# Kernel tuning notes

Hardware: AMD Instinct MI355X
Metric: run time of the kernel (lower is better)

The kernel has to match this reference:

```python
import jax, jax.numpy as jnp
import numpy as np

N, E, G, L = 50000, 800000, 256, 3
D, NF, EF, OUT = 300, 128, 16, 128
BN_EPS = 1e-5


def setup_inputs() -> dict:
    key = jax.random.key(0)
    ks = jax.random.split(key, 24)
    s = 0.02
    inp = {
        "node_feat": jax.random.normal(ks[0], (N, NF), jnp.float32),
        "edge_feat": jax.random.normal(ks[1], (E, EF), jnp.float32),
        "src": jax.random.randint(ks[2], (E,), 0, N),
        "dst": jax.random.randint(ks[3], (E,), 0, N),
        "graph_ids": jnp.sort(jax.random.randint(ks[4], (N,), 0, G)),
        "num_graphs": G,
        # encoder params
        "node_W": jax.random.normal(ks[5], (NF, D), jnp.float32) * s,
        "node_b": jnp.zeros((D,), jnp.float32),
        # per-layer edge encoders [L, EF, D]
        "edge_W": jax.random.normal(ks[6], (L, EF, D), jnp.float32) * s,
        "edge_b": jnp.zeros((L, D), jnp.float32),
        # per-layer GINEConv MLP: Linear(D,2D) BN ReLU Linear(2D,D) BN
        "W1": jax.random.normal(ks[7], (L, D, 2 * D), jnp.float32) * s,
        "b1": jnp.zeros((L, 2 * D), jnp.float32),
        "g1": jnp.ones((L, 2 * D), jnp.float32),
        "beta1": jnp.zeros((L, 2 * D), jnp.float32),
        "W2": jax.random.normal(ks[8], (L, 2 * D, D), jnp.float32) * s,
        "b2": jnp.zeros((L, D), jnp.float32),
        "g2": jnp.ones((L, D), jnp.float32),
        "beta2": jnp.zeros((L, D), jnp.float32),
        # prediction head
        "pred_W": jax.random.normal(ks[9], (D, OUT), jnp.float32) * s,
        "pred_b": jnp.zeros((OUT,), jnp.float32),
    }
    return inp


def _bn(x, g, b):
    # BatchNorm1d in training mode: biased batch statistics
    m = jnp.mean(x, axis=0)
    v = jnp.var(x, axis=0)
    return (x - m) * jax.lax.rsqrt(v + BN_EPS) * g + b


def reference(node_feat, edge_feat, src, dst, graph_ids, num_graphs,
              node_W, node_b, edge_W, edge_b,
              W1, b1, g1, beta1, W2, b2, g2, beta2,
              pred_W, pred_b):
    n_nodes = node_feat.shape[0]
    n_layers = edge_W.shape[0]
    hn = node_feat @ node_W + node_b  # [N, D]
    for l in range(n_layers):
        he = edge_feat @ edge_W[l] + edge_b[l]            # [E, D]
        msg = jax.nn.relu(hn[src] + he)                   # gather + edge fuse
        agg = jax.ops.segment_sum(msg, dst, num_segments=n_nodes)
        h = hn + agg                                      # (1+eps)*h + agg, eps=0
        h = jax.nn.relu(_bn(h @ W1[l] + b1[l], g1[l], beta1[l]))
        h = _bn(h @ W2[l] + b2[l], g2[l], beta2[l])
        hn = jax.nn.relu(h) if l != n_layers - 1 else h   # dropout p=0 -> identity
    # AvgPooling over nodes per graph
    cnt = jax.ops.segment_sum(jnp.ones((n_nodes, 1), hn.dtype), graph_ids,
                              num_segments=num_graphs)
    hg = jax.ops.segment_sum(hn, graph_ids, num_segments=num_graphs)
    hg = hg / jnp.maximum(cnt, 1.0)
    return hg @ pred_W + pred_b  # [G, OUT]
```

## Files before the change

kernel.cpp:

```cpp
#include <hip/hip_runtime.h>

#define N_NODES 50000
#define N_EDGES 800000
#define N_GRAPHS 256
#define N_LAYERS 3
#define DIM 300
#define NFEAT 128
#define EFEAT 16
#define OUTD 128
#define BN_EPS 1e-5f

typedef __attribute__((ext_vector_type(8))) short bfrag8;
typedef __attribute__((ext_vector_type(4))) float facc4;
typedef __attribute__((ext_vector_type(4))) unsigned short us4;
typedef __attribute__((ext_vector_type(8))) unsigned short us8;

__device__ __forceinline__ unsigned short f2bf(float f) {
    unsigned u = __float_as_uint(f);
    unsigned r = ((u >> 16) & 1u) + 0x7fffu;
    return (unsigned short)((u + r) >> 16);
}
__device__ __forceinline__ float bf2f(unsigned short h) {
    return __uint_as_float(((unsigned)h) << 16);
}
__device__ __forceinline__ void split2(float v, unsigned short& h, unsigned short& l) {
    h = f2bf(v);
    l = f2bf(v - bf2f(h));
}

__device__ __forceinline__ void load_lds16(const void* gsrc, void* ldsdst) {
    __builtin_amdgcn_global_load_lds(
        (const __attribute__((address_space(1))) unsigned int*)gsrc,
        (__attribute__((address_space(3))) unsigned int*)ldsdst,
        16, 0, 0);
}

#define MFMA16(a, b, c) __builtin_amdgcn_mfma_f32_16x16x32_bf16(a, b, c, 0, 0, 0)

__global__ __launch_bounds__(256) void tobf4(
    const float* __restrict__ x, unsigned short* __restrict__ H, int n4)
{
    int i = blockIdx.x * 256 + threadIdx.x;
    if (i >= n4) return;
    float4 v = ((const float4*)x)[i];
    us4 h;
    h.x = f2bf(v.x); h.y = f2bf(v.y); h.z = f2bf(v.z); h.w = f2bf(v.w);
    ((us4*)H)[i] = h;
}

__global__ __launch_bounds__(256) void conv_wt(
    const float* __restrict__ W, unsigned short* __restrict__ H,
    unsigned short* __restrict__ L, int K, int N, int Kp, int Np)
{
    int idx = blockIdx.x * 256 + threadIdx.x;
    if (idx >= Np * Kp) return;
    int n = idx / Kp;
    int k = idx - n * Kp;
    float v = (n < N && k < K) ? W[(size_t)k * N + n] : 0.f;
    unsigned short h, l;
    split2(v, h, l);
    H[idx] = h;
    L[idx] = l;
}

__global__ __launch_bounds__(256, 2) void gemm_pp(
    const unsigned short* __restrict__ Ah,
    const unsigned short* __restrict__ Bth, const unsigned short* __restrict__ Btl,
    const float* __restrict__ bias, float* __restrict__ C,
    int M, int N, int Kp, float* __restrict__ stats)
{
    __shared__ unsigned short lds[12288];
    const int tid = threadIdx.x;
    const int lane = tid & 63;
    const int w = tid >> 6;
    const int m0 = blockIdx.y * 128;
    const int n0 = blockIdx.x * 128;
    const int wm = (w & 1) * 64;
    const int wn = (w >> 1) * 64;

    const int srow = lane >> 2;
    const int scol = (lane & 3) * 8;

    const unsigned short* gp[6];
    unsigned loff[6];
#pragma unroll
    for (int i = 0; i < 6; ++i) {
        int c = w * 6 + i;
        const unsigned short* pl = (c < 8) ? Ah : (c < 16) ? Bth : Btl;
        int rowg;
        if (c < 8) {
            rowg = m0 + (c & 7) * 16 + srow;
            rowg = min(rowg, M - 1);
        } else {
            rowg = n0 + (c & 7) * 16 + srow;
        }
        gp[i] = pl + (size_t)rowg * Kp + scol;
        loff[i] = c * 512;
    }

    facc4 acc[4][4];
    facc4 zero = {0.f, 0.f, 0.f, 0.f};
#pragma unroll
    for (int i = 0; i < 4; ++i)
#pragma unroll
        for (int j = 0; j < 4; ++j) acc[i][j] = zero;

    const int fr = lane & 15;
    const int fq = (lane >> 4) * 8;

    for (int k0 = 0; k0 < Kp; k0 += 32) {
#pragma unroll
        for (int i = 0; i < 6; ++i) {
            load_lds16(gp[i], &lds[loff[i]]);
            gp[i] += 32;
        }
        __syncthreads();

        bfrag8 ah[4], bh[4], bl[4];
#pragma unroll
        for (int t = 0; t < 4; ++t) {
            int ar = wm + t * 16 + fr;
            ah[t] = *(const bfrag8*)&lds[ar * 32 + fq];
            int br = wn + t * 16 + fr;
            bh[t] = *(const bfrag8*)&lds[4096 + br * 32 + fq];
            bl[t] = *(const bfrag8*)&lds[8192 + br * 32 + fq];
        }
#pragma unroll
        for (int i = 0; i < 4; ++i)
#pragma unroll
            for (int j = 0; j < 4; ++j) {
                acc[i][j] = MFMA16(ah[i], bh[j], acc[i][j]);
                acc[i][j] = MFMA16(ah[i], bl[j], acc[i][j]);
            }
        __syncthreads();
    }

#pragma unroll
    for (int i = 0; i < 4; ++i)
#pragma unroll
        for (int j = 0; j < 4; ++j) {
            int col = n0 + wn + j * 16 + (lane & 15);
            if (col >= N) continue;
            float bv = bias[col];
#pragma unroll
            for (int r = 0; r < 4; ++r) {
                int row = m0 + wm + i * 16 + (lane >> 4) * 4 + r;
                if (row < M)
                    C[(size_t)row * N + col] = acc[i][j][r] + bv;
            }
        }

    if (stats != nullptr) {
#pragma unroll
        for (int j = 0; j < 4; ++j) {
            int col = n0 + wn + j * 16 + (lane & 15);
            float cs = 0.f, cq = 0.f;
            if (col < N) {
                float bv = bias[col];
#pragma unroll
                for (int i = 0; i < 4; ++i)
#pragma unroll
                    for (int r = 0; r < 4; ++r) {
                        int row = m0 + wm + i * 16 + (lane >> 4) * 4 + r;
                        if (row < M) {
                            float y = acc[i][j][r] + bv;
                            cs += y;
                            cq = fmaf(y, y, cq);
                        }
                    }
            }
            cs += __shfl_xor(cs, 16, 64); cq += __shfl_xor(cq, 16, 64);
            cs += __shfl_xor(cs, 32, 64); cq += __shfl_xor(cq, 32, 64);
            if ((lane >> 4) == 0 && col < N) {
                atomicAdd(&stats[col], cs);
                atomicAdd(&stats[N + col], cq);
            }
        }
    }
}

__global__ __launch_bounds__(256, 2) void gemm_af(
    const float* __restrict__ A, const unsigned short* __restrict__ Bth,
    const unsigned short* __restrict__ Btl, const float* __restrict__ bias,
    float* __restrict__ C, int M, int N, int K, int Kp,
    const float* __restrict__ abn, float* __restrict__ stats)
{
    __shared__ unsigned short lds[12288];
    const int tid = threadIdx.x;
    const int lane = tid & 63;
    const int w = tid >> 6;
    const int m0 = blockIdx.y * 128;
    const int n0 = blockIdx.x * 128;
    const int wm = (w & 1) * 64;
    const int wn = (w >> 1) * 64;

    const int srow = lane >> 2;
    const int scol = (lane & 3) * 8;

    const unsigned short* gpb[4];
    unsigned loffb[4];
#pragma unroll
    for (int i = 0; i < 4; ++i) {
        int c = w * 4 + i;
        const unsigned short* pl = (c < 8) ? Bth : Btl;
        int rowg = n0 + (c & 7) * 16 + srow;
        gpb[i] = pl + (size_t)rowg * Kp + scol;
        loffb[i] = 4096 + c * 512;
    }

    facc4 acc[4][4];
    facc4 zero = {0.f, 0.f, 0.f, 0.f};
#pragma unroll
    for (int i = 0; i < 4; ++i)
#pragma unroll
        for (int j = 0; j < 4; ++j) acc[i][j] = zero;

    const int fr = lane & 15;
    const int fq = (lane >> 4) * 8;

    for (int k0 = 0; k0 < Kp; k0 += 32) {
#pragma unroll
        for (int i = 0; i < 4; ++i) {
            load_lds16(gpb[i], &lds[loffb[i]]);
            gpb[i] += 32;
        }
#pragma unroll
        for (int i = 0; i < 4; ++i) {
            int idx = tid + i * 256;
            int row = idx >> 3;
            int q4 = idx & 7;
            int rg = min(m0 + row, M - 1);
            int kk = k0 + q4 * 4;
            us4 h;
            if (kk < K) {
                float4 v = *(const float4*)&A[(size_t)rg * K + kk];
                float4 sa = *(const float4*)&abn[kk];
                float4 sb = *(const float4*)&abn[K + kk];
                h.x = f2bf(fmaxf(fmaf(v.x, sa.x, sb.x), 0.f));
                h.y = f2bf(fmaxf(fmaf(v.y, sa.y, sb.y), 0.f));
                h.z = f2bf(fmaxf(fmaf(v.z, sa.z, sb.z), 0.f));
                h.w = f2bf(fmaxf(fmaf(v.w, sa.w, sb.w), 0.f));
            } else {
                h.x = 0; h.y = 0; h.z = 0; h.w = 0;
            }
            *(us4*)&lds[row * 32 + q4 * 4] = h;
        }
        __syncthreads();

        bfrag8 ah[4], bh[4], bl[4];
#pragma unroll
        for (int t = 0; t < 4; ++t) {
            int ar = wm + t * 16 + fr;
            ah[t] = *(const bfrag8*)&lds[ar * 32 + fq];
            int br = wn + t * 16 + fr;
            bh[t] = *(const bfrag8*)&lds[4096 + br * 32 + fq];
            bl[t] = *(const bfrag8*)&lds[8192 + br * 32 + fq];
        }
#pragma unroll
        for (int i = 0; i < 4; ++i)
#pragma unroll
            for (int j = 0; j < 4; ++j) {
                acc[i][j] = MFMA16(ah[i], bh[j], acc[i][j]);
                acc[i][j] = MFMA16(ah[i], bl[j], acc[i][j]);
            }
        __syncthreads();
    }

#pragma unroll
    for (int i = 0; i < 4; ++i)
#pragma unroll
        for (int j = 0; j < 4; ++j) {
            int col = n0 + wn + j * 16 + (lane & 15);
            if (col >= N) continue;
            float bv = bias[col];
#pragma unroll
            for (int r = 0; r < 4; ++r) {
                int row = m0 + wm + i * 16 + (lane >> 4) * 4 + r;
                if (row < M)
                    C[(size_t)row * N + col] = acc[i][j][r] + bv;
            }
        }

    if (stats != nullptr) {
#pragma unroll
        for (int j = 0; j < 4; ++j) {
            int col = n0 + wn + j * 16 + (lane & 15);
            float cs = 0.f, cq = 0.f;
            if (col < N) {
                float bv = bias[col];
#pragma unroll
                for (int i = 0; i < 4; ++i)
#pragma unroll
                    for (int r = 0; r < 4; ++r) {
                        int row = m0 + wm + i * 16 + (lane >> 4) * 4 + r;
                        if (row < M) {
                            float y = acc[i][j][r] + bv;
                            cs += y;
                            cq = fmaf(y, y, cq);
                        }
                    }
            }
            cs += __shfl_xor(cs, 16, 64); cq += __shfl_xor(cq, 16, 64);
            cs += __shfl_xor(cs, 32, 64); cq += __shfl_xor(cq, 32, 64);
            if ((lane >> 4) == 0 && col < N) {
                atomicAdd(&stats[col], cs);
                atomicAdd(&stats[N + col], cq);
            }
        }
    }
}

__global__ __launch_bounds__(256) void csr_count(const int* __restrict__ dst, int* __restrict__ P)
{
    int e = blockIdx.x * 256 + threadIdx.x;
    if (e < N_EDGES) atomicAdd(&P[dst[e] + 1], 1);
}

__global__ __launch_bounds__(1024) void csr_scan(int* __restrict__ P)
{
    __shared__ int part[1024];
    const int t = threadIdx.x;
    const int CH = 49;
    int i0 = t * CH;
    int s = 0;
    for (int i = i0; i < i0 + CH; ++i) {
        if (i <= N_NODES) { s += P[i]; P[i] = s; }
    }
    part[t] = s;
    __syncthreads();
    if (t == 0) {
        int run = 0;
        for (int k = 0; k < 1024; ++k) { int tmp = part[k]; part[k] = run; run += tmp; }
    }
    __syncthreads();
    int off = part[t];
    for (int i = i0; i < i0 + CH; ++i) {
        if (i <= N_NODES) P[i] += off;
    }
}

__global__ __launch_bounds__(256) void csr_fill(
    const int* __restrict__ dst, int* __restrict__ P, int* __restrict__ eids)
{
    int e = blockIdx.x * 256 + threadIdx.x;
    if (e < N_EDGES) {
        int pos = atomicAdd(&P[dst[e]], 1);
        eids[pos] = e;
    }
}

__global__ __launch_bounds__(256) void edge_pack_bf(
    const int* __restrict__ src, const int* __restrict__ eids,
    const float* __restrict__ edge_feat, int* __restrict__ es,
    unsigned short* __restrict__ efsb)
{
    int j = blockIdx.x * 256 + threadIdx.x;
    if (j >= N_EDGES) return;
    int e = eids[j];
    es[j] = src[e];
    const float* sp = edge_feat + (size_t)e * EFEAT;
    us8 o0, o1;
#pragma unroll
    for (int k = 0; k < 8; ++k) {
        o0[k] = f2bf(sp[k]);
        o1[k] = f2bf(sp[8 + k]);
    }
    *(us8*)&efsb[(size_t)j * EFEAT] = o0;
    *(us8*)&efsb[(size_t)j * EFEAT + 8] = o1;
}

__global__ __launch_bounds__(256) void gather_agg7(
    const float* __restrict__ hn, const unsigned short* __restrict__ efsb,
    const int* __restrict__ es, const int* __restrict__ P,
    const float* __restrict__ eW, const float* __restrict__ eb,
    unsigned short* __restrict__ aggH)
{
    const int v = blockIdx.x * 4 + (threadIdx.x >> 6);
    if (v >= N_NODES) return;
    const int lane = threadIdx.x & 63;

    float wr[EFEAT][5];
    float acc[5];
    float ebv[5];
#pragma unroll
    for (int c = 0; c < 5; ++c) {
        int d = lane + 64 * c;
        bool dv = d < DIM;
        acc[c] = dv ? hn[(size_t)v * DIM + d] : 0.f;
        ebv[c] = dv ? eb[d] : 0.f;
#pragma unroll
        for (int k = 0; k < EFEAT; ++k)
            wr[k][c] = dv ? eW[k * DIM + d] : 0.f;
    }

    const int j0 = (v == 0) ? 0 : P[v - 1];
    const int j1 = P[v];

    int j = j0;
    for (; j + 4 <= j1; j += 4) {
        int s0 = __builtin_amdgcn_readfirstlane(es[j]);
        int s1 = __builtin_amdgcn_readfirstlane(es[j + 1]);
        int s2 = __builtin_amdgcn_readfirstlane(es[j + 2]);
        int s3 = __builtin_amdgcn_readfirstlane(es[j + 3]);
        const float* __restrict__ h0 = hn + (size_t)s0 * DIM;
        const float* __restrict__ h1 = hn + (size_t)s1 * DIM;
        const float* __restrict__ h2p = hn + (size_t)s2 * DIM;
        const float* __restrict__ h3 = hn + (size_t)s3 * DIM;
        float hv[4][5];
#pragma unroll
        for (int c = 0; c < 5; ++c) {
            int d = lane + 64 * c;
            bool dv = d < DIM;
            hv[0][c] = dv ? h0[d] : 0.f;
            hv[1][c] = dv ? h1[d] : 0.f;
            hv[2][c] = dv ? h2p[d] : 0.f;
            hv[3][c] = dv ? h3[d] : 0.f;
        }
        us8 pk[4][2];
#pragma unroll
        for (int u = 0; u < 4; ++u) {
            pk[u][0] = *(const us8*)&efsb[(size_t)(j + u) * EFEAT];
            pk[u][1] = *(const us8*)&efsb[(size_t)(j + u) * EFEAT + 8];
        }
#pragma unroll
        for (int u = 0; u < 4; ++u) {
            float ef[EFEAT];
#pragma unroll
            for (int k = 0; k < 8; ++k) {
                ef[k] = bf2f(pk[u][0][k]);
                ef[8 + k] = bf2f(pk[u][1][k]);
            }
#pragma unroll
            for (int c = 0; c < 5; ++c) {
                float he = ebv[c];
#pragma unroll
                for (int k = 0; k < EFEAT; ++k) he = fmaf(ef[k], wr[k][c], he);
                acc[c] += fmaxf(hv[u][c] + he, 0.f);
            }
        }
    }
    for (; j < j1; ++j) {
        int s = __builtin_amdgcn_readfirstlane(es[j]);
        const float* __restrict__ hp = hn + (size_t)s * DIM;
        float hv[5];
#pragma unroll
        for (int c = 0; c < 5; ++c) {
            int d = lane + 64 * c;
            hv[c] = (d < DIM) ? hp[d] : 0.f;
        }
        us8 p0 = *(const us8*)&efsb[(size_t)j * EFEAT];
        us8 p1 = *(const us8*)&efsb[(size_t)j * EFEAT + 8];
        float ef[EFEAT];
#pragma unroll
        for (int k = 0; k < 8; ++k) {
            ef[k] = bf2f(p0[k]);
            ef[8 + k] = bf2f(p1[k]);
        }
#pragma unroll
        for (int c = 0; c < 5; ++c) {
            float he = ebv[c];
#pragma unroll
            for (int k = 0; k < EFEAT; ++k) he = fmaf(ef[k], wr[k][c], he);
            acc[c] += fmaxf(hv[c] + he, 0.f);
        }
    }

#pragma unroll
    for (int c = 0; c < 5; ++c)
        aggH[(size_t)v * 320 + lane + 64 * c] = f2bf(acc[c]);
}

__global__ __launch_bounds__(256) void bn_finalize(
    const float* __restrict__ stats, const float* __restrict__ g,
    const float* __restrict__ beta, float* __restrict__ ab, int C)
{
    int c = blockIdx.x * 256 + threadIdx.x;
    if (c >= C) return;
    const float invN = 1.f / (float)N_NODES;
    float m = stats[c] * invN;
    float v = stats[C + c] * invN - m * m;
    float a = g[c] * rsqrtf(v + BN_EPS);
    ab[c] = a;
    ab[C + c] = beta[c] - m * a;
}

__global__ __launch_bounds__(256) void bn_apply(
    const float* __restrict__ x, const float* __restrict__ ab,
    float* __restrict__ y, int total4, int C, int relu)
{
    int i = blockIdx.x * 256 + threadIdx.x;
    if (i >= total4) return;
    float4 v = ((const float4*)x)[i];
    int c = (i << 2) % C;
    const float* a = ab + c;
    const float* bb = ab + C + c;
    float4 r;
    r.x = fmaf(v.x, a[0], bb[0]);
    r.y = fmaf(v.y, a[1], bb[1]);
    r.z = fmaf(v.z, a[2], bb[2]);
    r.w = fmaf(v.w, a[3], bb[3]);
    if (relu) {
        r.x = fmaxf(r.x, 0.f); r.y = fmaxf(r.y, 0.f);
        r.z = fmaxf(r.z, 0.f); r.w = fmaxf(r.w, 0.f);
    }
    ((float4*)y)[i] = r;
}

__global__ __launch_bounds__(256) void pool_seg_bn(
    const float* __restrict__ h2, const int* __restrict__ gid,
    const float* __restrict__ ab, float* __restrict__ hg)
{
    const int g = blockIdx.x;
    int lo = 0, hi = N_NODES;
    while (lo < hi) { int mid = (lo + hi) >> 1; if (gid[mid] < g) lo = mid + 1; else hi = mid; }
    int lo2 = lo, hi2 = N_NODES;
    while (lo2 < hi2) { int mid = (lo2 + hi2) >> 1; if (gid[mid] < g + 1) lo2 = mid + 1; else hi2 = mid; }
    const float inv = 1.f / fmaxf((float)(lo2 - lo), 1.f);
    for (int d = threadIdx.x; d < DIM; d += 256) {
        float s = 0.f;
        for (int r = lo; r < lo2; ++r) s += h2[(size_t)r * DIM + d];
        hg[(size_t)g * DIM + d] = fmaf(s * inv, ab[d], ab[DIM + d]);
    }
}

#define TS 64
#define BK 16
#define ASP 68

__global__ __launch_bounds__(256) void sgemm_bias(
    const float* __restrict__ A, const float* __restrict__ B,
    const float* __restrict__ bias, float* __restrict__ C,
    int M, int Ncol, int K)
{
    __shared__ float As[BK][ASP];
    __shared__ float Bs[BK][TS];
    const int tid = threadIdx.x;
    const int bm = blockIdx.x * TS;
    const int bn = blockIdx.y * TS;
    const int tm = (tid >> 4) * 4;
    const int tn = (tid & 15) * 4;
    float acc[4][4] = {};

    for (int k0 = 0; k0 < K; k0 += BK) {
#pragma unroll
        for (int i = 0; i < 4; ++i) {
            int idx = tid + i * 256;
            int m = idx >> 4;
            int k = idx & 15;
            int row = bm + m, kk = k0 + k;
            float v = 0.f;
            if (row < M && kk < K) v = A[(size_t)row * K + kk];
            As[k][m] = v;
        }
#pragma unroll
        for (int i = 0; i < 4; ++i) {
            int idx = tid + i * 256;
            int k = idx >> 6;
            int n = idx & 63;
            int col = bn + n, kk = k0 + k;
            float v = 0.f;
            if (col < Ncol && kk < K) v = B[(size_t)kk * Ncol + col];
            Bs[k][n] = v;
        }
        __syncthreads();
#pragma unroll
        for (int k = 0; k < BK; ++k) {
            float4 av = *(const float4*)&As[k][tm];
            float4 bv = *(const float4*)&Bs[k][tn];
            float a4[4] = {av.x, av.y, av.z, av.w};
            float b4[4] = {bv.x, bv.y, bv.z, bv.w};
#pragma unroll
            for (int i = 0; i < 4; ++i)
#pragma unroll
                for (int j = 0; j < 4; ++j)
                    acc[i][j] = fmaf(a4[i], b4[j], acc[i][j]);
        }
        __syncthreads();
    }

#pragma unroll
    for (int i = 0; i < 4; ++i) {
        int row = bm + tm + i;
        if (row >= M) continue;
#pragma unroll
        for (int j = 0; j < 4; ++j) {
            int col = bn + tn + j;
            if (col < Ncol)
                C[(size_t)row * Ncol + col] = acc[i][j] + bias[col];
        }
    }
}

extern "C" void kernel_launch(void* const* d_in, const int* in_sizes, int n_in,
                              void* d_out, int out_size, void* d_ws, size_t ws_size,
                              hipStream_t stream)
{
    const float* node_feat = (const float*)d_in[0];
    const float* edge_feat = (const float*)d_in[1];
    const int*   src       = (const int*)d_in[2];
    const int*   dst       = (const int*)d_in[3];
    const int*   gid       = (const int*)d_in[4];
    const float* node_W = (const float*)d_in[6];
    const float* node_b = (const float*)d_in[7];
    const float* edge_W = (const float*)d_in[8];
    const float* edge_b = (const float*)d_in[9];
    const float* W1  = (const float*)d_in[10];
    const float* b1  = (const float*)d_in[11];
    const float* g1  = (const float*)d_in[12];
    const float* be1 = (const float*)d_in[13];
    const float* W2  = (const float*)d_in[14];
    const float* b2  = (const float*)d_in[15];
    const float* g2  = (const float*)d_in[16];
    const float* be2 = (const float*)d_in[17];
    const float* pred_W = (const float*)d_in[18];
    const float* pred_b = (const float*)d_in[19];
    float* out = (float*)d_out;

    char* base = (char*)d_ws;
    float* hn            = (float*)(base + 0);
    float* h2            = hn;
    float* x1            = (float*)(base + 60000000);
    unsigned short* nfH  = (unsigned short*)x1;
    unsigned short* aggH = (unsigned short*)(base + 180000000);
    int*   es            = (int*)(base + 212000000);
    unsigned short* efsb = (unsigned short*)(base + 215200000);
    unsigned short* wtH  = (unsigned short*)(base + 244000000);
    unsigned short* wtL  = (unsigned short*)(base + 244500000);
    int*   eids          = (int*)(base + 245000000);
    int*   P             = (int*)(base + 248200000);
    float* stats         = (float*)(base + 248400016);
    float* ab            = (float*)(base + 248407216);
    float* hg            = (float*)(base + 248414416);
    float* stats2        = stats + 1200;
    float* ab2           = ab + 1200;

    dim3 blk(256);

    tobf4<<<dim3((N_NODES * NFEAT / 4 + 255) / 256), blk, 0, stream>>>(
        node_feat, nfH, N_NODES * NFEAT / 4);
    conv_wt<<<dim3((384 * 128 + 255) / 256), blk, 0, stream>>>(
        node_W, wtH, wtL, NFEAT, DIM, 128, 384);
    gemm_pp<<<dim3(3, 391), blk, 0, stream>>>(
        nfH, wtH, wtL, node_b, hn, N_NODES, DIM, 128, nullptr);

    hipMemsetAsync(P, 0, (N_NODES + 1) * sizeof(int), stream);
    csr_count<<<dim3((N_EDGES + 255) / 256), blk, 0, stream>>>(dst, P);
    csr_scan<<<dim3(1), dim3(1024), 0, stream>>>(P);
    csr_fill<<<dim3((N_EDGES + 255) / 256), blk, 0, stream>>>(dst, P, eids);
    edge_pack_bf<<<dim3((N_EDGES + 255) / 256), blk, 0, stream>>>(
        src, eids, edge_feat, es, efsb);

    for (int l = 0; l < N_LAYERS; ++l) {
        gather_agg7<<<dim3((N_NODES + 3) / 4), blk, 0, stream>>>(
            hn, efsb, es, P,
            edge_W + (size_t)l * EFEAT * DIM, edge_b + (size_t)l * DIM, aggH);

        hipMemsetAsync(stats, 0, 1800 * sizeof(float), stream);

        conv_wt<<<dim3((640 * 320 + 255) / 256), blk, 0, stream>>>(
            W1 + (size_t)l * DIM * 2 * DIM, wtH, wtL, DIM, 2 * DIM, 320, 640);
        gemm_pp<<<dim3(5, 391), blk, 0, stream>>>(
            aggH, wtH, wtL, b1 + (size_t)l * 2 * DIM, x1,
            N_NODES, 2 * DIM, 320, stats);
        bn_finalize<<<dim3(3), blk, 0, stream>>>(
            stats, g1 + (size_t)l * 2 * DIM, be1 + (size_t)l * 2 * DIM, ab, 2 * DIM);

        conv_wt<<<dim3((384 * 608 + 255) / 256), blk, 0, stream>>>(
            W2 + (size_t)l * 2 * DIM * DIM, wtH, wtL, 2 * DIM, DIM, 608, 384);
        gemm_af<<<dim3(3, 391), blk, 0, stream>>>(
            x1, wtH, wtL, b2 + (size_t)l * DIM, h2, N_NODES, DIM, 2 * DIM, 608,
            ab, stats2);
        bn_finalize<<<dim3(2), blk, 0, stream>>>(
            stats2, g2 + (size_t)l * DIM, be2 + (size_t)l * DIM, ab2, DIM);

        if (l < N_LAYERS - 1)
            bn_apply<<<dim3((N_NODES * DIM / 4 + 255) / 256), blk, 0, stream>>>(
                h2, ab2, hn, N_NODES * DIM / 4, DIM, 1);
    }

    pool_seg_bn<<<dim3(N_GRAPHS), blk, 0, stream>>>(h2, gid, ab2, hg);
    sgemm_bias<<<dim3((N_GRAPHS + 63) / 64, (OUTD + 63) / 64), blk, 0, stream>>>(
        hg, pred_W, pred_b, out, N_GRAPHS, OUTD, DIM);
}
```

Measured before the change: 1.974 ms.

## Compute edge encoder in gather via MFMA with split-bf16 weights in LDS

Replaces the scalar per-lane FMA edge-encoder in the gather/aggregate kernel with MFMA 16x16 bf16 ops. The edge weights and bias are packed into hi/lo bf16 fragments (bias folded in as a 17th input column set to 1) and staged in LDS. Each wave now processes 16 destination nodes, working through edges in tiles of 16. Invalid rows read from a dummy buffer of -1e30 so the ReLU zeroes them. The aim is to offload the 16-wide dot-product FLOPs to matrix cores. The cost is scattered per-row hn gathers with a 16-column stride instead of coalesced lane-contiguous loads, plus wasted MFMA work on nodes with few edges.

```diff
diff --git a/kernel.cpp b/kernel.cpp
--- a/kernel.cpp
+++ b/kernel.cpp
@@ -61,6 +61,39 @@
     split2(v, h, l);
     H[idx] = h;
     L[idx] = l;
+}
+
+__global__ __launch_bounds__(256) void conv_ew(
+    const float* __restrict__ eW, const float* __restrict__ eb,
+    unsigned short* __restrict__ out)
+{
+    int t = blockIdx.x * 256 + threadIdx.x;
+    if (t >= 2432) return;
+    int c = t >> 7;
+    int p = (t >> 6) & 1;
+    int lane = t & 63;
+    int n = lane & 15, g = lane >> 4;
+    int col = c * 16 + n;
+    us8 o;
+#pragma unroll
+    for (int i = 0; i < 8; ++i) {
+        int k = 8 * g + i;
+        float v = 0.f;
+        if (col < DIM) {
+            if (k < EFEAT) v = eW[k * DIM + col];
+            else if (k == EFEAT) v = eb[col];
+        }
+        unsigned short h, l;
+        split2(v, h, l);
+        o[i] = p ? l : h;
+    }
+    *(us8*)&out[(size_t)t * 8] = o;
+}
+
+__global__ __launch_bounds__(256) void fill_dummy(float* __restrict__ d)
+{
+    int i = blockIdx.x * 256 + threadIdx.x;
+    if (i < 320) d[i] = -1e30f;
 }
 
 __global__ __launch_bounds__(256, 2) void gemm_pp(
@@ -369,105 +402,88 @@
     *(us8*)&efsb[(size_t)j * EFEAT + 8] = o1;
 }
 
-__global__ __launch_bounds__(256) void gather_agg7(
+__global__ __launch_bounds__(256, 3) void gather_mf(
     const float* __restrict__ hn, const unsigned short* __restrict__ efsb,
     const int* __restrict__ es, const int* __restrict__ P,
-    const float* __restrict__ eW, const float* __restrict__ eb,
+    const unsigned short* __restrict__ eWf, const float* __restrict__ dummy,
     unsigned short* __restrict__ aggH)
 {
-    const int v = blockIdx.x * 4 + (threadIdx.x >> 6);
-    if (v >= N_NODES) return;
-    const int lane = threadIdx.x & 63;
-
-    float wr[EFEAT][5];
-    float acc[5];
-    float ebv[5];
-#pragma unroll
-    for (int c = 0; c < 5; ++c) {
-        int d = lane + 64 * c;
-        bool dv = d < DIM;
-        acc[c] = dv ? hn[(size_t)v * DIM + d] : 0.f;
-        ebv[c] = dv ? eb[d] : 0.f;
-#pragma unroll
-        for (int k = 0; k < EFEAT; ++k)
-            wr[k][c] = dv ? eW[k * DIM + d] : 0.f;
-    }
-
-    const int j0 = (v == 0) ? 0 : P[v - 1];
-    const int j1 = P[v];
-
-    int j = j0;
-    for (; j + 4 <= j1; j += 4) {
-        int s0 = __builtin_amdgcn_readfirstlane(es[j]);
-        int s1 = __builtin_amdgcn_readfirstlane(es[j + 1]);
-        int s2 = __builtin_amdgcn_readfirstlane(es[j + 2]);
-        int s3 = __builtin_amdgcn_readfirstlane(es[j + 3]);
-        const float* __restrict__ h0 = hn + (size_t)s0 * DIM;
-        const float* __restrict__ h1 = hn + (size_t)s1 * DIM;
-        const float* __restrict__ h2p = hn + (size_t)s2 * DIM;
-        const float* __restrict__ h3 = hn + (size_t)s3 * DIM;
-        float hv[4][5];
-#pragma unroll
-        for (int c = 0; c < 5; ++c) {
-            int d = lane + 64 * c;
-            bool dv = d < DIM;
-            hv[0][c] = dv ? h0[d] : 0.f;
-            hv[1][c] = dv ? h1[d] : 0.f;
-            hv[2][c] = dv ? h2p[d] : 0.f;
-            hv[3][c] = dv ? h3[d] : 0.f;
-        }
-        us8 pk[4][2];
-#pragma unroll
-        for (int u = 0; u < 4; ++u) {
-            pk[u][0] = *(const us8*)&efsb[(size_t)(j + u) * EFEAT];
-            pk[u][1] = *(const us8*)&efsb[(size_t)(j + u) * EFEAT + 8];
-        }
-#pragma unroll
-        for (int u = 0; u < 4; ++u) {
-            float ef[EFEAT];
-#pragma unroll
-            for (int k = 0; k < 8; ++k) {
-                ef[k] = bf2f(pk[u][0][k]);
-                ef[8 + k] = bf2f(pk[u][1][k]);
-            }
-#pragma unroll
-            for (int c = 0; c < 5; ++c) {
-                float he = ebv[c];
-#pragma unroll
-                for (int k = 0; k < EFEAT; ++k) he = fmaf(ef[k], wr[k][c], he);
-                acc[c] += fmaxf(hv[u][c] + he, 0.f);
-            }
-        }
-    }
-    for (; j < j1; ++j) {
-        int s = __builtin_amdgcn_readfirstlane(es[j]);
-        const float* __restrict__ hp = hn + (size_t)s * DIM;
-        float hv[5];
-#pragma unroll
-        for (int c = 0; c < 5; ++c) {
-            int d = lane + 64 * c;
-            hv[c] = (d < DIM) ? hp[d] : 0.f;
-        }
-        us8 p0 = *(const us8*)&efsb[(size_t)j * EFEAT];
-        us8 p1 = *(const us8*)&efsb[(size_t)j * EFEAT + 8];
-        float ef[EFEAT];
-#pragma unroll
-        for (int k = 0; k < 8; ++k) {
-            ef[k] = bf2f(p0[k]);
-            ef[8 + k] = bf2f(p1[k]);
-        }
-#pragma unroll
-        for (int c = 0; c < 5; ++c) {
-            float he = ebv[c];
-#pragma unroll
-            for (int k = 0; k < EFEAT; ++k) he = fmaf(ef[k], wr[k][c], he);
-            acc[c] += fmaxf(hv[c] + he, 0.f);
-        }
-    }
-
-#pragma unroll
-    for (int c = 0; c < 5; ++c)
-        aggH[(size_t)v * 320 + lane + 64 * c] = f2bf(acc[c]);
+    __shared__ unsigned short ldsw[19456];
+    const int tid = threadIdx.x;
+    const int lane = tid & 63;
+    const int w = tid >> 6;
+
+#pragma unroll
+    for (int it = 0; it < 10; ++it) {
+        int i = tid + it * 256;
+        if (i < 2432) load_lds16(eWf + (size_t)i * 8, &ldsw[i * 8]);
+    }
+    __syncthreads();
+
+    const int n15 = lane & 15;
+    const int g = lane >> 4;
+    const int r0 = g * 4;
+    const int wid = blockIdx.x * 4 + w;
+
+    for (int t = 0; t < 16; ++t) {
+        const int v = wid * 16 + t;
+        if (v >= N_NODES) return;
+        const int j0 = (v == 0) ? 0 : P[v - 1];
+        const int j1 = P[v];
+
+        facc4 zero4 = {0.f, 0.f, 0.f, 0.f};
+        facc4 acc[19];
+#pragma unroll
+        for (int c = 0; c < 19; ++c) acc[c] = zero4;
+
+        for (int jb = j0; jb < j1; jb += 16) {
+            bfrag8 af = {0, 0, 0, 0, 0, 0, 0, 0};
+            if (g < 2) {
+                int eA = min(jb + n15, N_EDGES - 1);
+                af = *(const bfrag8*)&efsb[(size_t)eA * EFEAT + 8 * g];
+            } else if (g == 2) {
+                af[0] = (short)0x3F80;
+            }
+            const float* ptr[4];
+#pragma unroll
+            for (int r = 0; r < 4; ++r) {
+                int e = jb + r0 + r;
+                int s = es[min(e, N_EDGES - 1)];
+                ptr[r] = (e < j1) ? (hn + (size_t)s * DIM + n15) : (dummy + n15);
+            }
+#pragma unroll
+            for (int c = 0; c < 19; ++c) {
+                bfrag8 bh = *(const bfrag8*)&ldsw[(c * 128 + lane) * 8];
+                bfrag8 bl = *(const bfrag8*)&ldsw[(c * 128 + 64 + lane) * 8];
+                facc4 tt = MFMA16(af, bl, zero4);
+                tt = MFMA16(af, bh, tt);
+#pragma unroll
+                for (int r = 0; r < 4; ++r) {
+                    float hv = ptr[r][c * 16];
+                    acc[c][r] += fmaxf(tt[r] + hv, 0.f);
+                }
+            }
+        }
+
+        float s[19];
+#pragma unroll
+        for (int c = 0; c < 19; ++c) {
+            float x = acc[c][0] + acc[c][1] + acc[c][2] + acc[c][3];
+            x += __shfl_xor(x, 16, 64);
+            x += __shfl_xor(x, 32, 64);
+            s[c] = x;
+        }
+#pragma unroll
+        for (int m = 0; m < 5; ++m) {
+            int d = lane + 64 * m;
+            float val = (g == 0) ? s[(4 * m     < 19) ? 4 * m     : 18]
+                      : (g == 1) ? s[(4 * m + 1 < 19) ? 4 * m + 1 : 18]
+                      : (g == 2) ? s[(4 * m + 2 < 19) ? 4 * m + 2 : 18]
+                                 : s[(4 * m + 3 < 19) ? 4 * m + 3 : 18];
+            float o = (d < DIM) ? (val + hn[(size_t)v * DIM + d]) : 0.f;
+            aggH[(size_t)v * 320 + d] = f2bf(o);
+        }
+    }
 }
 
 __global__ __launch_bounds__(256) void bn_finalize(
@@ -624,9 +640,11 @@
     unsigned short* aggH = (unsigned short*)(base + 180000000);
     int*   es            = (int*)(base + 212000000);
     unsigned short* efsb = (unsigned short*)(base + 215200000);
+    float* dummy         = (float*)(base + 243900000);
     unsigned short* wtH  = (unsigned short*)(base + 244000000);
     unsigned short* wtL  = (unsigned short*)(base + 244500000);
     int*   eids          = (int*)(base + 245000000);
+    unsigned short* eWf  = (unsigned short*)(base + 245000000);
     int*   P             = (int*)(base + 248200000);
     float* stats         = (float*)(base + 248400016);
     float* ab            = (float*)(base + 248407216);
@@ -649,11 +667,13 @@
     csr_fill<<<dim3((N_EDGES + 255) / 256), blk, 0, stream>>>(dst, P, eids);
     edge_pack_bf<<<dim3((N_EDGES + 255) / 256), blk, 0, stream>>>(
         src, eids, edge_feat, es, efsb);
+    fill_dummy<<<dim3(2), blk, 0, stream>>>(dummy);
 
     for (int l = 0; l < N_LAYERS; ++l) {
-        gather_agg7<<<dim3((N_NODES + 3) / 4), blk, 0, stream>>>(
-            hn, efsb, es, P,
-            edge_W + (size_t)l * EFEAT * DIM, edge_b + (size_t)l * DIM, aggH);
+        conv_ew<<<dim3(10), blk, 0, stream>>>(
+            edge_W + (size_t)l * EFEAT * DIM, edge_b + (size_t)l * DIM, eWf);
+        gather_mf<<<dim3(782), blk, 0, stream>>>(
+            hn, efsb, es, P, eWf, dummy, aggH);
 
         hipMemsetAsync(stats, 0, 1800 * sizeof(float), stream);
 
```

Result: slower. 4.457 ms (+125.8%).
